# Performance work log

Measured on AMD Instinct MI355X. Metric: run time of the kernel, lower is better.

Reference implementation:

```python
import jax, jax.numpy as jnp
import numpy as np

N = 50000        # nodes
E = 1_600_000    # edges (avg degree 32)
H = 4            # attention heads
DPH = 32         # dims per head
D = H * DPH      # hidden/output dim = 128
IN_DIM = 5
NEG_SLOPE = 0.2
LN_EPS = 1e-5


def _glorot(key, shape):
    fan_in = shape[0] if len(shape) > 1 else shape[-1]
    return jax.random.normal(key, shape, jnp.float32) / jnp.sqrt(jnp.float32(fan_in))


def setup_inputs() -> dict:
    key = jax.random.key(0)
    ks = jax.random.split(key, 24)
    inp = {
        'x': jax.random.normal(ks[0], (N, IN_DIM), jnp.float32),
        'w_in': _glorot(ks[1], (IN_DIM, D)),
        'b_in': jnp.zeros((D,), jnp.float32),
    }
    for i in range(3):
        k = 2 + 6 * i
        inp[f'w{i}'] = _glorot(ks[k], (D, D))            # GAT linear
        inp[f'asrc{i}'] = _glorot(ks[k + 1], (H, DPH))   # att_src
        inp[f'adst{i}'] = _glorot(ks[k + 2], (H, DPH))   # att_dst
        inp[f'cb{i}'] = jnp.zeros((D,), jnp.float32)     # conv bias
        inp[f'g{i}'] = jnp.ones((D,), jnp.float32)       # LN gamma
        inp[f'lb{i}'] = jnp.zeros((D,), jnp.float32)     # LN beta
    inp['edge_index'] = jax.random.randint(ks[23], (2, E), 0, N, dtype=jnp.int32)
    return inp


def _gat_layer(h, src, dst, W, a_src, a_dst, bias):
    # h: [N, D]; src/dst: [E+N] (self loops included)
    xh = (h @ W).reshape(N, H, DPH)                      # [N, H, DPH]
    al_s = jnp.einsum('nhd,hd->nh', xh, a_src)           # [N, H]
    al_d = jnp.einsum('nhd,hd->nh', xh, a_dst)
    e = jax.nn.leaky_relu(al_s[src] + al_d[dst], NEG_SLOPE)   # [E', H]
    m = jax.ops.segment_max(e, dst, num_segments=N)      # segment softmax over incoming edges
    ex = jnp.exp(e - m[dst])
    denom = jax.ops.segment_sum(ex, dst, num_segments=N)
    alpha = ex / (denom[dst] + 1e-16)                    # [E', H]
    out = jax.ops.segment_sum(xh[src] * alpha[..., None], dst, num_segments=N)
    return out.reshape(N, D) + bias


def _layer_norm(x, g, b):
    mu = jnp.mean(x, axis=-1, keepdims=True)
    var = jnp.mean((x - mu) ** 2, axis=-1, keepdims=True)
    return (x - mu) * jax.lax.rsqrt(var + LN_EPS) * g + b


def reference(x, w_in, b_in,
              w0, asrc0, adst0, cb0, g0, lb0,
              w1, asrc1, adst1, cb1, g1, lb1,
              w2, asrc2, adst2, cb2, g2, lb2,
              edge_index):
    loops = jnp.arange(N, dtype=edge_index.dtype)
    src = jnp.concatenate([edge_index[0], loops])        # PyG GATConv add_self_loops=True
    dst = jnp.concatenate([edge_index[1], loops])
    h = x @ w_in + b_in                                  # [N, D]
    layers = [(w0, asrc0, adst0, cb0, g0, lb0),
              (w1, asrc1, adst1, cb1, g1, lb1),
              (w2, asrc2, adst2, cb2, g2, lb2)]
    for i, (W, a_s, a_d, cb, g, lb) in enumerate(layers):
        h_new = _gat_layer(h, src, dst, W, a_s, a_d, cb)
        h_new = _layer_norm(h_new, g, lb)
        if i < 2:
            h_new = jax.nn.relu(h_new)                   # dropout = identity in eval
        h = h + h_new                                    # dims always match (128)
    return h
```

## Files before the change

kernel.cpp:

```cpp
#include <hip/hip_runtime.h>

#define NN 50000
#define NE 1600000
#define EP (NE + NN)
#define D 128
#define H 4
#define NEG 0.2f
#define LN_EPS 1e-5f
#define NBUCK 49
#define BCAP 40960
#define CHUNK 4096

typedef _Float16 f16;
typedef _Float16 half8 __attribute__((ext_vector_type(8)));
typedef _Float16 half2v __attribute__((ext_vector_type(2)));
typedef float f32x4v __attribute__((ext_vector_type(4)));
typedef unsigned short u16;
typedef unsigned int u32;

static __device__ __forceinline__ float leakyf(float v) { return fmaxf(v, NEG * v); }

static __device__ __forceinline__ int fkey(float v) {
    int b = __float_as_int(v);
    return b >= 0 ? b : (b ^ 0x7fffffff);
}
static __device__ __forceinline__ float fdec(int k) {
    return __int_as_float(k >= 0 ? k : (k ^ 0x7fffffff));
}
#define NEG_INF_KEY 0x807fffff

__global__ void k_init(int* __restrict__ deg, int* __restrict__ gmaxk,
                       int* __restrict__ gcur,
                       const float* __restrict__ w0, const float* __restrict__ w1,
                       const float* __restrict__ w2, f16* __restrict__ wt,
                       const float* __restrict__ as0, const float* __restrict__ ad0,
                       const float* __restrict__ as1, const float* __restrict__ ad1,
                       const float* __restrict__ as2, const float* __restrict__ ad2,
                       f16* __restrict__ ws16) {
    int t = blockIdx.x * blockDim.x + threadIdx.x;
    if (t < NN) deg[t] = 0;
    if (t < 12) gmaxk[t] = NEG_INF_KEY;
    if (t < NBUCK) gcur[t] = 0;
    int u = t - 50176;
    if (u >= 0 && u < 3 * D * D) {
        int l = u / (D * D), rem = u % (D * D);
        int k = rem >> 7, c = rem & 127;
        const float* w = (l == 0) ? w0 : (l == 1) ? w1 : w2;
        wt[l * D * D + c * D + k] = (f16)w[rem];
    }
    int v = t - 99328;
    if (v >= 0 && v < 3 * 16 * D) {
        int l = v / (16 * D), rem = v % (16 * D);
        int c = rem >> 7, k = rem & 127;
        f16 out = (f16)0.f;
        if (c < 8) {
            int head = c >> 1;
            const float* w = (l == 0) ? w0 : (l == 1) ? w1 : w2;
            const float* av = (c & 1) ? ((l == 0) ? ad0 : (l == 1) ? ad1 : ad2)
                                      : ((l == 0) ? as0 : (l == 1) ? as1 : as2);
            float s = 0.f;
#pragma unroll
            for (int j = 0; j < 32; j++)
                s = fmaf(w[k * D + head * 32 + j], av[head * 32 + j], s);
            out = (f16)s;
        }
        ws16[l * 16 * D + c * D + k] = out;
    }
}

__global__ __launch_bounds__(256) void k_bin(const int* __restrict__ ei,
                                             int* __restrict__ gcur,
                                             u32* __restrict__ binned) {
    __shared__ u32 pk[CHUNK];
    __shared__ int hist[NBUCK], base[NBUCK], lcur[NBUCK];
    int tid = threadIdx.x;
    int cbase = blockIdx.x * CHUNK;
    if (tid < NBUCK) hist[tid] = 0;
    __syncthreads();
#pragma unroll
    for (int j = 0; j < CHUNK / 256; j++) {
        int k = cbase + j * 256 + tid;
        u32 v = 0xFFFFFFFFu;
        if (k < EP) {
            int src, dst;
            if (k < NE) { src = ei[k]; dst = ei[NE + k]; }
            else        { src = k - NE; dst = src; }
            v = ((u32)dst << 16) | (u32)src;
            atomicAdd(&hist[dst >> 10], 1);
        }
        pk[j * 256 + tid] = v;
    }
    __syncthreads();
    if (tid < NBUCK) {
        base[tid] = atomicAdd(&gcur[tid], hist[tid]);
        lcur[tid] = 0;
    }
    __syncthreads();
#pragma unroll
    for (int j = 0; j < CHUNK / 256; j++) {
        u32 v = pk[j * 256 + tid];
        if (v != 0xFFFFFFFFu) {
            int b = v >> 26;
            int pos = base[b] + atomicAdd(&lcur[b], 1);
            binned[(size_t)b * BCAP + pos] = v;
        }
    }
}

__global__ __launch_bounds__(1024) void k_cnt2(const int* __restrict__ gcur,
                                               const u32* __restrict__ binned,
                                               int* __restrict__ deg) {
    __shared__ int hist[1024];
    int b = blockIdx.x >> 2, sub = blockIdx.x & 3;
    hist[threadIdx.x] = 0;
    __syncthreads();
    int cnt = gcur[b];
    const u32* bb = binned + (size_t)b * BCAP;
    for (int i = sub * 1024 + threadIdx.x; i < cnt; i += 4096)
        atomicAdd(&hist[(bb[i] >> 16) & 1023], 1);
    __syncthreads();
    int n = (b << 10) + threadIdx.x;
    if (n < NN && hist[threadIdx.x]) atomicAdd(&deg[n], hist[threadIdx.x]);
}

#define SCAN_B 512
__global__ void k_scan1(const int* __restrict__ deg, int* __restrict__ stmp, int* __restrict__ bsum) {
    __shared__ int sm[SCAN_B];
    int i = blockIdx.x * SCAN_B + threadIdx.x;
    sm[threadIdx.x] = (i < NN) ? ((deg[i] + 3) & ~3) : 0;
    __syncthreads();
    for (int off = 1; off < SCAN_B; off <<= 1) {
        int t = (threadIdx.x >= off) ? sm[threadIdx.x - off] : 0;
        __syncthreads();
        sm[threadIdx.x] += t;
        __syncthreads();
    }
    if (i < NN) stmp[i] = sm[threadIdx.x];
    if (threadIdx.x == SCAN_B - 1) bsum[blockIdx.x] = sm[SCAN_B - 1];
}

__global__ void k_scan2(int* __restrict__ bsum, int nb) {
    __shared__ int sm[256];
    int v = (threadIdx.x < nb) ? bsum[threadIdx.x] : 0;
    sm[threadIdx.x] = v;
    __syncthreads();
    for (int off = 1; off < 256; off <<= 1) {
        int t = (threadIdx.x >= off) ? sm[threadIdx.x - off] : 0;
        __syncthreads();
        sm[threadIdx.x] += t;
        __syncthreads();
    }
    if (threadIdx.x < nb) bsum[threadIdx.x] = sm[threadIdx.x];
}

__global__ void k_scan3(const int* __restrict__ stmp, const int* __restrict__ bsum, int* __restrict__ rowptr) {
    int i = blockIdx.x * SCAN_B + threadIdx.x;
    if (i >= NN) return;
    int add = (blockIdx.x > 0) ? bsum[blockIdx.x - 1] : 0;
    rowptr[i + 1] = stmp[i] + add;
    if (i == 0) rowptr[0] = 0;
}

__global__ void k_pad(const int* __restrict__ rowptr, const int* __restrict__ deg,
                      int* __restrict__ cur, u16* __restrict__ csr) {
    int i = blockIdx.x * blockDim.x + threadIdx.x;
    if (i >= NN) return;
    int rp = rowptr[i];
    cur[i] = rp;
    int d = deg[i];
    int ad = (d + 3) & ~3;
    for (int j = d; j < ad; ++j) csr[rp + j] = 0xFFFFu;
}

__global__ __launch_bounds__(1024) void k_scatter(const int* __restrict__ gcur,
                                                  int* __restrict__ cur,
                                                  const u32* __restrict__ binned,
                                                  u16* __restrict__ csr) {
    int b = blockIdx.x >> 2, sub = blockIdx.x & 3;
    int cnt = gcur[b];
    const u32* bb = binned + (size_t)b * BCAP;
    for (int i = sub * 1024 + threadIdx.x; i < cnt; i += 4096) {
        u32 v = bb[i];
        int dst = v >> 16;
        int pos = atomicAdd(&cur[dst], 1);
        csr[pos] = (u16)(v & 0xFFFFu);
    }
}

__global__ void k_in(const float* __restrict__ x, const float* __restrict__ w,
                     const float* __restrict__ b, f16* __restrict__ h16) {
    int t = blockIdx.x * blockDim.x + threadIdx.x;
    if (t >= NN * D) return;
    int n = t >> 7, d = t & 127;
    const float* xr = x + n * 5;
    float acc = b[d];
#pragma unroll
    for (int k = 0; k < 5; k++) acc = fmaf(xr[k], w[k * D + d], acc);
    h16[t] = (f16)acc;
}

__global__ __launch_bounds__(256) void k_gemm(const f16* __restrict__ h16,
                                              const f16* __restrict__ wt,
                                              const f16* __restrict__ ws16,
                                              f16* __restrict__ xh,
                                              float* __restrict__ als,
                                              float* __restrict__ ald,
                                              int* __restrict__ gmaxk) {
    __shared__ int sgk[4];
    if (threadIdx.x < 4) sgk[threadIdx.x] = NEG_INF_KEY;
    int wid = threadIdx.x >> 6;
    int lane = threadIdx.x & 63;
    int wbase = blockIdx.x * 128 + wid * 32;
    int r = lane & 15;
    int g = lane >> 4;

    int arow0 = wbase + r;      if (arow0 >= NN) arow0 = NN - 1;
    int arow1 = wbase + 16 + r; if (arow1 >= NN) arow1 = NN - 1;
    const f16* a0p = h16 + (size_t)arow0 * D + g * 8;
    const f16* a1p = h16 + (size_t)arow1 * D + g * 8;

    f32x4v acc0[8], acc1[8], al0, al1;
#pragma unroll
    for (int nt = 0; nt < 8; nt++) {
        acc0[nt] = (f32x4v){0.f, 0.f, 0.f, 0.f};
        acc1[nt] = (f32x4v){0.f, 0.f, 0.f, 0.f};
    }
    al0 = (f32x4v){0.f, 0.f, 0.f, 0.f};
    al1 = (f32x4v){0.f, 0.f, 0.f, 0.f};

#pragma unroll
    for (int ks = 0; ks < 4; ks++) {
        half8 a0 = *(const half8*)(a0p + ks * 32);
        half8 a1 = *(const half8*)(a1p + ks * 32);
        half8 bal = *(const half8*)(ws16 + (size_t)r * D + ks * 32 + g * 8);
        al0 = __builtin_amdgcn_mfma_f32_16x16x32_f16(a0, bal, al0, 0, 0, 0);
        al1 = __builtin_amdgcn_mfma_f32_16x16x32_f16(a1, bal, al1, 0, 0, 0);
#pragma unroll
        for (int nt = 0; nt < 8; nt++) {
            half8 b = *(const half8*)(wt + (size_t)(nt * 16 + r) * D + ks * 32 + g * 8);
            acc0[nt] = __builtin_amdgcn_mfma_f32_16x16x32_f16(a0, b, acc0[nt], 0, 0, 0);
            acc1[nt] = __builtin_amdgcn_mfma_f32_16x16x32_f16(a1, b, acc1[nt], 0, 0, 0);
        }
    }

#pragma unroll
    for (int rg = 0; rg < 4; rg++) {
        int n0 = wbase + g * 4 + rg;
        if (n0 < NN) {
#pragma unroll
            for (int nt = 0; nt < 8; nt++)
                xh[(size_t)n0 * D + nt * 16 + r] = (f16)acc0[nt][rg];
        }
        int n1 = wbase + 16 + g * 4 + rg;
        if (n1 < NN) {
#pragma unroll
            for (int nt = 0; nt < 8; nt++)
                xh[(size_t)n1 * D + nt * 16 + r] = (f16)acc1[nt][rg];
        }
    }

    float m = -1e30f;
#pragma unroll
    for (int rg = 0; rg < 4; rg++) {
        int n0 = wbase + g * 4 + rg;
        int n1 = wbase + 16 + g * 4 + rg;
        float v0 = al0[rg], v1 = al1[rg];
        if (r < 8) {
            int hh = r >> 1;
            if (r & 1) {
                if (n0 < NN) ald[n0 * H + hh] = v0;
                if (n1 < NN) ald[n1 * H + hh] = v1;
            } else {
                if (n0 < NN) als[n0 * H + hh] = v0;
                if (n1 < NN) als[n1 * H + hh] = v1;
                m = fmaxf(m, fmaxf(v0, v1));
            }
        }
    }
    m = fmaxf(m, __shfl_xor(m, 16));
    m = fmaxf(m, __shfl_xor(m, 32));
    __syncthreads();
    if (lane < 8 && !(r & 1)) atomicMax(&sgk[r >> 1], fkey(m));
    __syncthreads();
    if (threadIdx.x < 4) atomicMax(&gmaxk[threadIdx.x], sgk[threadIdx.x]);
}

__global__ __launch_bounds__(256) void k_agg(const f16* __restrict__ xh,
                                             const float* __restrict__ als,
                                             const float* __restrict__ ald,
                                             const int* __restrict__ gmaxk,
                                             const int* __restrict__ rowptr,
                                             const u16* __restrict__ csr,
                                             const float* __restrict__ cb,
                                             const float* __restrict__ gamma,
                                             const float* __restrict__ beta,
                                             f16* __restrict__ h16,
                                             float* __restrict__ hout, int do_relu) {
    int node = blockIdx.x * 4 + (threadIdx.x >> 6);
    if (node >= NN) return;
    int lane = threadIdx.x & 63;
    int slot = lane >> 4;
    int q = lane & 15;
    int head = q >> 2;

    int start = rowptr[node], end = rowptr[node + 1];

    float adH = ald[node * H + head];
    float mH = leakyf(fdec(gmaxk[head]) + adH);

    float acc[8];
#pragma unroll
    for (int j = 0; j < 8; j++) acc[j] = 0.f;
    float den = 0.f;

    int sh = (slot & 1) << 4;
    bool hiw = (slot & 2) != 0;

#pragma unroll 4
    for (int e = start; e < end; e += 4) {
        uint2 cw = *(const uint2*)(csr + e);
        unsigned dw = hiw ? cw.y : cw.x;
        unsigned s = (dw >> sh) & 0xffffu;
        bool valid = s != 0xffffu;
        unsigned sc = valid ? s : 0u;
        float al = als[sc * H + head];
        float ev = valid ? __expf(leakyf(al + adH) - mH) : 0.f;
        den += ev;
        half8 p = *(const half8*)(xh + sc * D + q * 8);
#pragma unroll
        for (int j = 0; j < 8; j++) acc[j] = fmaf(ev, (float)p[j], acc[j]);
    }

    den += __shfl_xor(den, 16);
    den += __shfl_xor(den, 32);
#pragma unroll
    for (int j = 0; j < 8; j++) {
        acc[j] += __shfl_xor(acc[j], 16);
        acc[j] += __shfl_xor(acc[j], 32);
    }

    float inv_den = 1.f / (den + 1e-16f);
    float o[8];
    const float4* cb4 = (const float4*)(cb + q * 8);
    float4 cba = cb4[0], cbb = cb4[1];
    o[0] = fmaf(acc[0], inv_den, cba.x);
    o[1] = fmaf(acc[1], inv_den, cba.y);
    o[2] = fmaf(acc[2], inv_den, cba.z);
    o[3] = fmaf(acc[3], inv_den, cba.w);
    o[4] = fmaf(acc[4], inv_den, cbb.x);
    o[5] = fmaf(acc[5], inv_den, cbb.y);
    o[6] = fmaf(acc[6], inv_den, cbb.z);
    o[7] = fmaf(acc[7], inv_den, cbb.w);

    float s = 0.f;
#pragma unroll
    for (int j = 0; j < 8; j++) s += o[j];
#pragma unroll
    for (int off = 1; off < 16; off <<= 1) s += __shfl_xor(s, off);
    float mean = s * (1.f / 128.f);
    float v = 0.f;
    float c[8];
#pragma unroll
    for (int j = 0; j < 8; j++) { c[j] = o[j] - mean; v = fmaf(c[j], c[j], v); }
#pragma unroll
    for (int off = 1; off < 16; off <<= 1) v += __shfl_xor(v, off);
    float inv = rsqrtf(v * (1.f / 128.f) + LN_EPS);

    int dim = q * 8 + slot * 2;
    float2 g2 = *(const float2*)(gamma + dim);
    float2 b2 = *(const float2*)(beta + dim);
    float r0 = c[slot * 2] * inv * g2.x + b2.x;
    float r1 = c[slot * 2 + 1] * inv * g2.y + b2.y;
    if (do_relu) { r0 = fmaxf(r0, 0.f); r1 = fmaxf(r1, 0.f); }
    half2v hv16 = *(const half2v*)&h16[(size_t)node * D + dim];
    float n0 = (float)hv16[0] + r0;
    float n1 = (float)hv16[1] + r1;
    if (do_relu) {
        half2v h2; h2[0] = (f16)n0; h2[1] = (f16)n1;
        *(half2v*)&h16[(size_t)node * D + dim] = h2;
    } else {
        float2* hp = (float2*)&hout[(size_t)node * D + dim];
        *hp = (float2){n0, n1};
    }
}

extern "C" void kernel_launch(void* const* d_in, const int* in_sizes, int n_in,
                              void* d_out, int out_size, void* d_ws, size_t ws_size,
                              hipStream_t stream) {
    const float* x    = (const float*)d_in[0];
    const float* w_in = (const float*)d_in[1];
    const float* b_in = (const float*)d_in[2];
    const int*   ei   = (const int*)d_in[21];
    float* hout = (float*)d_out;

    char* w = (char*)d_ws;
    int* deg    = (int*)w;  w += (size_t)NN * 4;
    int* cur    = (int*)w;  w += (size_t)NN * 4;
    int* stmp   = (int*)w;  w += (size_t)NN * 4;
    int* bsum   = (int*)w;  w += 1024;
    int* rowptr = (int*)w;  w += (size_t)(NN + 4) * 4;
    int* gmaxk  = (int*)w;  w += 64;
    int* gcur   = (int*)w;  w += 256;
    u16* csr    = (u16*)w;  w += (size_t)(EP + 3 * NN + 16) * 2;
    f16* h16    = (f16*)w;  w += (size_t)NN * D * 2;
    f16* xh     = (f16*)w;  w += (size_t)NN * D * 2;
    f16* wt     = (f16*)w;  w += (size_t)3 * D * D * 2;
    f16* ws16   = (f16*)w;  w += (size_t)3 * 16 * D * 2;
    float* als  = (float*)w; w += (size_t)NN * H * 4;
    float* ald  = (float*)w; w += (size_t)NN * H * 4;
    u32* binned = (u32*)h16;

    k_init<<<412, 256, 0, stream>>>(deg, gmaxk, gcur,
                                    (const float*)d_in[3], (const float*)d_in[9],
                                    (const float*)d_in[15], wt,
                                    (const float*)d_in[4], (const float*)d_in[5],
                                    (const float*)d_in[10], (const float*)d_in[11],
                                    (const float*)d_in[16], (const float*)d_in[17],
                                    ws16);
    k_bin<<<(EP + CHUNK - 1) / CHUNK, 256, 0, stream>>>(ei, gcur, binned);
    k_cnt2<<<NBUCK * 4, 1024, 0, stream>>>(gcur, binned, deg);
    int nbScan = (NN + SCAN_B - 1) / SCAN_B;
    k_scan1<<<nbScan, SCAN_B, 0, stream>>>(deg, stmp, bsum);
    k_scan2<<<1, 256, 0, stream>>>(bsum, nbScan);
    k_scan3<<<nbScan, SCAN_B, 0, stream>>>(stmp, bsum, rowptr);
    k_pad<<<(NN + 255) / 256, 256, 0, stream>>>(rowptr, deg, cur, csr);
    k_scatter<<<NBUCK * 4, 1024, 0, stream>>>(gcur, cur, binned, csr);

    k_in<<<(NN * D) / 256, 256, 0, stream>>>(x, w_in, b_in, h16);

    for (int L = 0; L < 3; ++L) {
        const float* cb   = (const float*)d_in[6 + 6 * L];
        const float* g    = (const float*)d_in[7 + 6 * L];
        const float* lb   = (const float*)d_in[8 + 6 * L];
        k_gemm<<<(NN + 127) / 128, 256, 0, stream>>>(h16, wt + (size_t)L * D * D,
                                                     ws16 + (size_t)L * 16 * D,
                                                     xh, als, ald, gmaxk + 4 * L);
        k_agg<<<NN / 4, 256, 0, stream>>>(xh, als, ald, gmaxk + 4 * L, rowptr, csr,
                                          cb, g, lb, h16, hout, L < 2 ? 1 : 0);
    }
}
```

Measured before the change: 411.6 us.

## Partition CSR by source chunk and aggregate multiple nodes per wave chunk-wise

```diff
diff --git a/kernel.cpp b/kernel.cpp
--- a/kernel.cpp
+++ b/kernel.cpp
@@ -10,9 +10,14 @@
 #define NBUCK 49
 #define BCAP 40960
 #define CHUNK 4096
+#define NCHUNK 8
+#define CSH 13
+#define NSEG (NN * NCHUNK)
+#define NPW 8
 
 typedef _Float16 f16;
 typedef _Float16 half8 __attribute__((ext_vector_type(8)));
+typedef _Float16 half4 __attribute__((ext_vector_type(4)));
 typedef _Float16 half2v __attribute__((ext_vector_type(2)));
 typedef float f32x4v __attribute__((ext_vector_type(4)));
 typedef unsigned short u16;
@@ -29,7 +34,7 @@
 }
 #define NEG_INF_KEY 0x807fffff
 
-__global__ void k_init(int* __restrict__ deg, int* __restrict__ gmaxk,
+__global__ void k_init(int* __restrict__ deg8, int* __restrict__ gmaxk,
                        int* __restrict__ gcur,
                        const float* __restrict__ w0, const float* __restrict__ w1,
                        const float* __restrict__ w2, f16* __restrict__ wt,
@@ -38,7 +43,7 @@
                        const float* __restrict__ as2, const float* __restrict__ ad2,
                        f16* __restrict__ ws16) {
     int t = blockIdx.x * blockDim.x + threadIdx.x;
-    if (t < NN) deg[t] = 0;
+    if (t < NSEG) deg8[t] = 0;
     if (t < 12) gmaxk[t] = NEG_INF_KEY;
     if (t < NBUCK) gcur[t] = 0;
     int u = t - 50176;
@@ -109,25 +114,34 @@
 
 __global__ __launch_bounds__(1024) void k_cnt2(const int* __restrict__ gcur,
                                                const u32* __restrict__ binned,
-                                               int* __restrict__ deg) {
-    __shared__ int hist[1024];
+                                               int* __restrict__ deg8) {
+    __shared__ int hist[1024 * NCHUNK];
     int b = blockIdx.x >> 2, sub = blockIdx.x & 3;
-    hist[threadIdx.x] = 0;
+#pragma unroll
+    for (int j = 0; j < NCHUNK; j++) hist[j * 1024 + threadIdx.x] = 0;
     __syncthreads();
     int cnt = gcur[b];
     const u32* bb = binned + (size_t)b * BCAP;
-    for (int i = sub * 1024 + threadIdx.x; i < cnt; i += 4096)
-        atomicAdd(&hist[(bb[i] >> 16) & 1023], 1);
-    __syncthreads();
-    int n = (b << 10) + threadIdx.x;
-    if (n < NN && hist[threadIdx.x]) atomicAdd(&deg[n], hist[threadIdx.x]);
-}
-
-#define SCAN_B 512
-__global__ void k_scan1(const int* __restrict__ deg, int* __restrict__ stmp, int* __restrict__ bsum) {
+    for (int i = sub * 1024 + threadIdx.x; i < cnt; i += 4096) {
+        u32 v = bb[i];
+        int idx = (int)((v >> 16) & 1023) * NCHUNK + (int)((v & 0xffffu) >> CSH);
+        atomicAdd(&hist[idx], 1);
+    }
+    __syncthreads();
+    int nb0 = b << 10;
+    for (int i = threadIdx.x; i < 1024 * NCHUNK; i += 1024) {
+        int node = nb0 + (i >> 3);
+        int hv = hist[i];
+        if (node < NN && hv) atomicAdd(&deg8[node * NCHUNK + (i & 7)], hv);
+    }
+}
+
+#define SCAN_B 1024
+__global__ __launch_bounds__(1024) void k_scan1(const int* __restrict__ deg8,
+                                                int* __restrict__ stmp, int* __restrict__ bsum) {
     __shared__ int sm[SCAN_B];
     int i = blockIdx.x * SCAN_B + threadIdx.x;
-    sm[threadIdx.x] = (i < NN) ? ((deg[i] + 3) & ~3) : 0;
+    sm[threadIdx.x] = (i < NSEG) ? ((deg8[i] + 1) & ~1) : 0;
     __syncthreads();
     for (int off = 1; off < SCAN_B; off <<= 1) {
         int t = (threadIdx.x >= off) ? sm[threadIdx.x - off] : 0;
@@ -135,16 +149,16 @@
         sm[threadIdx.x] += t;
         __syncthreads();
     }
-    if (i < NN) stmp[i] = sm[threadIdx.x];
+    if (i < NSEG) stmp[i] = sm[threadIdx.x];
     if (threadIdx.x == SCAN_B - 1) bsum[blockIdx.x] = sm[SCAN_B - 1];
 }
 
-__global__ void k_scan2(int* __restrict__ bsum, int nb) {
-    __shared__ int sm[256];
+__global__ __launch_bounds__(1024) void k_scan2(int* __restrict__ bsum, int nb) {
+    __shared__ int sm[1024];
     int v = (threadIdx.x < nb) ? bsum[threadIdx.x] : 0;
     sm[threadIdx.x] = v;
     __syncthreads();
-    for (int off = 1; off < 256; off <<= 1) {
+    for (int off = 1; off < 1024; off <<= 1) {
         int t = (threadIdx.x >= off) ? sm[threadIdx.x - off] : 0;
         __syncthreads();
         sm[threadIdx.x] += t;
@@ -153,22 +167,23 @@
     if (threadIdx.x < nb) bsum[threadIdx.x] = sm[threadIdx.x];
 }
 
-__global__ void k_scan3(const int* __restrict__ stmp, const int* __restrict__ bsum, int* __restrict__ rowptr) {
+__global__ __launch_bounds__(1024) void k_scan3(const int* __restrict__ stmp,
+                                                const int* __restrict__ bsum, int* __restrict__ rowptr) {
     int i = blockIdx.x * SCAN_B + threadIdx.x;
-    if (i >= NN) return;
+    if (i >= NSEG) return;
     int add = (blockIdx.x > 0) ? bsum[blockIdx.x - 1] : 0;
     rowptr[i + 1] = stmp[i] + add;
     if (i == 0) rowptr[0] = 0;
 }
 
-__global__ void k_pad(const int* __restrict__ rowptr, const int* __restrict__ deg,
+__global__ void k_pad(const int* __restrict__ rowptr, const int* __restrict__ deg8,
                       int* __restrict__ cur, u16* __restrict__ csr) {
     int i = blockIdx.x * blockDim.x + threadIdx.x;
-    if (i >= NN) return;
+    if (i >= NSEG) return;
     int rp = rowptr[i];
     cur[i] = rp;
-    int d = deg[i];
-    int ad = (d + 3) & ~3;
+    int d = deg8[i];
+    int ad = (d + 1) & ~1;
     for (int j = d; j < ad; ++j) csr[rp + j] = 0xFFFFu;
 }
 
@@ -182,8 +197,9 @@
     for (int i = sub * 1024 + threadIdx.x; i < cnt; i += 4096) {
         u32 v = bb[i];
         int dst = v >> 16;
-        int pos = atomicAdd(&cur[dst], 1);
-        csr[pos] = (u16)(v & 0xFFFFu);
+        int src = v & 0xffffu;
+        int pos = atomicAdd(&cur[dst * NCHUNK + (src >> CSH)], 1);
+        csr[pos] = (u16)src;
     }
 }
 
@@ -285,102 +301,111 @@
     if (threadIdx.x < 4) atomicMax(&gmaxk[threadIdx.x], sgk[threadIdx.x]);
 }
 
-__global__ __launch_bounds__(256) void k_agg(const f16* __restrict__ xh,
-                                             const float* __restrict__ als,
-                                             const float* __restrict__ ald,
-                                             const int* __restrict__ gmaxk,
-                                             const int* __restrict__ rowptr,
-                                             const u16* __restrict__ csr,
-                                             const float* __restrict__ cb,
-                                             const float* __restrict__ gamma,
-                                             const float* __restrict__ beta,
-                                             f16* __restrict__ h16,
-                                             float* __restrict__ hout, int do_relu) {
-    int node = blockIdx.x * 4 + (threadIdx.x >> 6);
-    if (node >= NN) return;
+__global__ __launch_bounds__(256, 6) void k_agg(const f16* __restrict__ xh,
+                                                const float* __restrict__ als,
+                                                const float* __restrict__ ald,
+                                                const int* __restrict__ gmaxk,
+                                                const int* __restrict__ rp,
+                                                const u16* __restrict__ csr,
+                                                const float* __restrict__ cb,
+                                                const float* __restrict__ gamma,
+                                                const float* __restrict__ beta,
+                                                f16* __restrict__ h16,
+                                                float* __restrict__ hout, int do_relu) {
+    int wid = threadIdx.x >> 6;
     int lane = threadIdx.x & 63;
-    int slot = lane >> 4;
-    int q = lane & 15;
-    int head = q >> 2;
-
-    int start = rowptr[node], end = rowptr[node + 1];
-
-    float adH = ald[node * H + head];
-    float mH = leakyf(fdec(gmaxk[head]) + adH);
-
-    float acc[8];
-#pragma unroll
-    for (int j = 0; j < 8; j++) acc[j] = 0.f;
-    float den = 0.f;
-
-    int sh = (slot & 1) << 4;
-    bool hiw = (slot & 2) != 0;
-
-#pragma unroll 4
-    for (int e = start; e < end; e += 4) {
-        uint2 cw = *(const uint2*)(csr + e);
-        unsigned dw = hiw ? cw.y : cw.x;
-        unsigned s = (dw >> sh) & 0xffffu;
-        bool valid = s != 0xffffu;
-        unsigned sc = valid ? s : 0u;
-        float al = als[sc * H + head];
-        float ev = valid ? __expf(leakyf(al + adH) - mH) : 0.f;
-        den += ev;
-        half8 p = *(const half8*)(xh + sc * D + q * 8);
-#pragma unroll
-        for (int j = 0; j < 8; j++) acc[j] = fmaf(ev, (float)p[j], acc[j]);
-    }
-
-    den += __shfl_xor(den, 16);
-    den += __shfl_xor(den, 32);
-#pragma unroll
-    for (int j = 0; j < 8; j++) {
-        acc[j] += __shfl_xor(acc[j], 16);
-        acc[j] += __shfl_xor(acc[j], 32);
-    }
-
-    float inv_den = 1.f / (den + 1e-16f);
-    float o[8];
-    const float4* cb4 = (const float4*)(cb + q * 8);
-    float4 cba = cb4[0], cbb = cb4[1];
-    o[0] = fmaf(acc[0], inv_den, cba.x);
-    o[1] = fmaf(acc[1], inv_den, cba.y);
-    o[2] = fmaf(acc[2], inv_den, cba.z);
-    o[3] = fmaf(acc[3], inv_den, cba.w);
-    o[4] = fmaf(acc[4], inv_den, cbb.x);
-    o[5] = fmaf(acc[5], inv_den, cbb.y);
-    o[6] = fmaf(acc[6], inv_den, cbb.z);
-    o[7] = fmaf(acc[7], inv_den, cbb.w);
-
-    float s = 0.f;
-#pragma unroll
-    for (int j = 0; j < 8; j++) s += o[j];
-#pragma unroll
-    for (int off = 1; off < 16; off <<= 1) s += __shfl_xor(s, off);
-    float mean = s * (1.f / 128.f);
-    float v = 0.f;
-    float c[8];
-#pragma unroll
-    for (int j = 0; j < 8; j++) { c[j] = o[j] - mean; v = fmaf(c[j], c[j], v); }
-#pragma unroll
-    for (int off = 1; off < 16; off <<= 1) v += __shfl_xor(v, off);
-    float inv = rsqrtf(v * (1.f / 128.f) + LN_EPS);
-
-    int dim = q * 8 + slot * 2;
-    float2 g2 = *(const float2*)(gamma + dim);
-    float2 b2 = *(const float2*)(beta + dim);
-    float r0 = c[slot * 2] * inv * g2.x + b2.x;
-    float r1 = c[slot * 2 + 1] * inv * g2.y + b2.y;
-    if (do_relu) { r0 = fmaxf(r0, 0.f); r1 = fmaxf(r1, 0.f); }
-    half2v hv16 = *(const half2v*)&h16[(size_t)node * D + dim];
-    float n0 = (float)hv16[0] + r0;
-    float n1 = (float)hv16[1] + r1;
-    if (do_relu) {
-        half2v h2; h2[0] = (f16)n0; h2[1] = (f16)n1;
-        *(half2v*)&h16[(size_t)node * D + dim] = h2;
-    } else {
-        float2* hp = (float2*)&hout[(size_t)node * D + dim];
-        *hp = (float2){n0, n1};
+    int nbase = (blockIdx.x * 4 + wid) * NPW;
+    int slot = lane >> 5;
+    int q = lane & 31;
+    int head = q >> 3;
+    int sh = slot << 4;
+
+    float acc[NPW][4];
+    float den[NPW];
+#pragma unroll
+    for (int n = 0; n < NPW; n++) {
+        den[n] = 0.f;
+        acc[n][0] = acc[n][1] = acc[n][2] = acc[n][3] = 0.f;
+    }
+
+    float gm = fdec(gmaxk[head]);
+
+    for (int p = 0; p < 7; ++p) {
+#pragma unroll
+        for (int n = 0; n < NPW; n++) {
+            int node = nbase + n;
+            if (node >= NN) continue;
+            float adH = ald[node * H + head];
+            float mH = leakyf(gm + adH);
+            int seg = node * NCHUNK + p;
+            int s0 = rp[seg], s1 = rp[seg + 1];
+            for (int e = s0; e < s1; e += 2) {
+                u32 cw = *(const u32*)(csr + e);
+                unsigned s = (cw >> sh) & 0xffffu;
+                bool valid = s != 0xffffu;
+                unsigned sc = valid ? s : 0u;
+                float al = als[sc * H + head];
+                float ev = valid ? __expf(leakyf(al + adH) - mH) : 0.f;
+                den[n] += ev;
+                half4 pv = *(const half4*)(xh + (size_t)sc * D + q * 4);
+                acc[n][0] = fmaf(ev, (float)pv[0], acc[n][0]);
+                acc[n][1] = fmaf(ev, (float)pv[1], acc[n][1]);
+                acc[n][2] = fmaf(ev, (float)pv[2], acc[n][2]);
+                acc[n][3] = fmaf(ev, (float)pv[3], acc[n][3]);
+            }
+        }
+    }
+
+    float4 cb4 = ((const float4*)cb)[q];
+    float4 g4 = ((const float4*)gamma)[q];
+    float4 b4 = ((const float4*)beta)[q];
+
+#pragma unroll
+    for (int n = 0; n < NPW; n++) {
+        int node = nbase + n;
+        if (node >= NN) continue;
+        float d = den[n] + __shfl_xor(den[n], 32);
+        float o0 = acc[n][0] + __shfl_xor(acc[n][0], 32);
+        float o1 = acc[n][1] + __shfl_xor(acc[n][1], 32);
+        float o2 = acc[n][2] + __shfl_xor(acc[n][2], 32);
+        float o3 = acc[n][3] + __shfl_xor(acc[n][3], 32);
+        float inv_den = 1.f / (d + 1e-16f);
+        o0 = fmaf(o0, inv_den, cb4.x);
+        o1 = fmaf(o1, inv_den, cb4.y);
+        o2 = fmaf(o2, inv_den, cb4.z);
+        o3 = fmaf(o3, inv_den, cb4.w);
+
+        float s = o0 + o1 + o2 + o3;
+#pragma unroll
+        for (int off = 1; off < 32; off <<= 1) s += __shfl_xor(s, off);
+        float mean = s * (1.f / 128.f);
+        float c0 = o0 - mean, c1 = o1 - mean, c2 = o2 - mean, c3 = o3 - mean;
+        float v = c0 * c0 + c1 * c1 + c2 * c2 + c3 * c3;
+#pragma unroll
+        for (int off = 1; off < 32; off <<= 1) v += __shfl_xor(v, off);
+        float inv = rsqrtf(v * (1.f / 128.f) + LN_EPS);
+
+        float r0 = c0 * inv * g4.x + b4.x;
+        float r1 = c1 * inv * g4.y + b4.y;
+        float r2 = c2 * inv * g4.z + b4.z;
+        float r3 = c3 * inv * g4.w + b4.w;
+        if (do_relu) {
+            r0 = fmaxf(r0, 0.f); r1 = fmaxf(r1, 0.f);
+            r2 = fmaxf(r2, 0.f); r3 = fmaxf(r3, 0.f);
+        }
+        if (slot == 0) {
+            half4 hv = *(const half4*)&h16[(size_t)node * D + q * 4];
+            float n0 = (float)hv[0] + r0;
+            float n1 = (float)hv[1] + r1;
+            float n2 = (float)hv[2] + r2;
+            float n3 = (float)hv[3] + r3;
+            if (do_relu) {
+                half4 h2; h2[0] = (f16)n0; h2[1] = (f16)n1; h2[2] = (f16)n2; h2[3] = (f16)n3;
+                *(half4*)&h16[(size_t)node * D + q * 4] = h2;
+            } else {
+                *(float4*)&hout[(size_t)node * D + q * 4] = (float4){n0, n1, n2, n3};
+            }
+        }
     }
 }
 
@@ -394,14 +419,14 @@
     float* hout = (float*)d_out;
 
     char* w = (char*)d_ws;
-    int* deg    = (int*)w;  w += (size_t)NN * 4;
-    int* cur    = (int*)w;  w += (size_t)NN * 4;
-    int* stmp   = (int*)w;  w += (size_t)NN * 4;
-    int* bsum   = (int*)w;  w += 1024;
-    int* rowptr = (int*)w;  w += (size_t)(NN + 4) * 4;
+    int* deg8   = (int*)w;  w += (size_t)NSEG * 4;
+    int* cur    = (int*)w;  w += (size_t)NSEG * 4;
+    int* stmp   = (int*)w;  w += (size_t)NSEG * 4;
+    int* bsum   = (int*)w;  w += 4096;
+    int* rowptr = (int*)w;  w += (size_t)(NSEG + 8) * 4;
     int* gmaxk  = (int*)w;  w += 64;
     int* gcur   = (int*)w;  w += 256;
-    u16* csr    = (u16*)w;  w += (size_t)(EP + 3 * NN + 16) * 2;
+    u16* csr    = (u16*)w;  w += (size_t)(EP + NSEG + 64) * 2;
     f16* h16    = (f16*)w;  w += (size_t)NN * D * 2;
     f16* xh     = (f16*)w;  w += (size_t)NN * D * 2;
     f16* wt     = (f16*)w;  w += (size_t)3 * D * D * 2;
@@ -410,24 +435,25 @@
     float* ald  = (float*)w; w += (size_t)NN * H * 4;
     u32* binned = (u32*)h16;
 
-    k_init<<<412, 256, 0, stream>>>(deg, gmaxk, gcur,
-                                    (const float*)d_in[3], (const float*)d_in[9],
-                                    (const float*)d_in[15], wt,
-                                    (const float*)d_in[4], (const float*)d_in[5],
-                                    (const float*)d_in[10], (const float*)d_in[11],
-                                    (const float*)d_in[16], (const float*)d_in[17],
-                                    ws16);
+    k_init<<<1563, 256, 0, stream>>>(deg8, gmaxk, gcur,
+                                     (const float*)d_in[3], (const float*)d_in[9],
+                                     (const float*)d_in[15], wt,
+                                     (const float*)d_in[4], (const float*)d_in[5],
+                                     (const float*)d_in[10], (const float*)d_in[11],
+                                     (const float*)d_in[16], (const float*)d_in[17],
+                                     ws16);
     k_bin<<<(EP + CHUNK - 1) / CHUNK, 256, 0, stream>>>(ei, gcur, binned);
-    k_cnt2<<<NBUCK * 4, 1024, 0, stream>>>(gcur, binned, deg);
-    int nbScan = (NN + SCAN_B - 1) / SCAN_B;
-    k_scan1<<<nbScan, SCAN_B, 0, stream>>>(deg, stmp, bsum);
-    k_scan2<<<1, 256, 0, stream>>>(bsum, nbScan);
+    k_cnt2<<<NBUCK * 4, 1024, 0, stream>>>(gcur, binned, deg8);
+    int nbScan = (NSEG + SCAN_B - 1) / SCAN_B;
+    k_scan1<<<nbScan, SCAN_B, 0, stream>>>(deg8, stmp, bsum);
+    k_scan2<<<1, 1024, 0, stream>>>(bsum, nbScan);
     k_scan3<<<nbScan, SCAN_B, 0, stream>>>(stmp, bsum, rowptr);
-    k_pad<<<(NN + 255) / 256, 256, 0, stream>>>(rowptr, deg, cur, csr);
+    k_pad<<<(NSEG + 255) / 256, 256, 0, stream>>>(rowptr, deg8, cur, csr);
     k_scatter<<<NBUCK * 4, 1024, 0, stream>>>(gcur, cur, binned, csr);
 
     k_in<<<(NN * D) / 256, 256, 0, stream>>>(x, w_in, b_in, h16);
 
+    int aggBlocks = (NN + 4 * NPW - 1) / (4 * NPW);
     for (int L = 0; L < 3; ++L) {
         const float* cb   = (const float*)d_in[6 + 6 * L];
         const float* g    = (const float*)d_in[7 + 6 * L];
@@ -435,7 +461,7 @@
         k_gemm<<<(NN + 127) / 128, 256, 0, stream>>>(h16, wt + (size_t)L * D * D,
                                                      ws16 + (size_t)L * 16 * D,
                                                      xh, als, ald, gmaxk + 4 * L);
-        k_agg<<<NN / 4, 256, 0, stream>>>(xh, als, ald, gmaxk + 4 * L, rowptr, csr,
-                                          cb, g, lb, h16, hout, L < 2 ? 1 : 0);
-    }
-}
+        k_agg<<<aggBlocks, 256, 0, stream>>>(xh, als, ald, gmaxk + 4 * L, rowptr, csr,
+                                             cb, g, lb, h16, hout, L < 2 ? 1 : 0);
+    }
+}
```

Measured after the change: 1.054 ms. +156.0%, slower.

## Split each node's CSR row into source-range segments for gather locality

Applied to the files above, without the earlier changes.

```diff
diff --git a/kernel.cpp b/kernel.cpp
--- a/kernel.cpp
+++ b/kernel.cpp
@@ -10,6 +10,9 @@
 #define NBUCK 49
 #define BCAP 40960
 #define CHUNK 4096
+#define NCHUNK 4
+#define CSH 14
+#define NSEG (NN * NCHUNK)
 
 typedef _Float16 f16;
 typedef _Float16 half8 __attribute__((ext_vector_type(8)));
@@ -38,7 +41,7 @@
                        const float* __restrict__ as2, const float* __restrict__ ad2,
                        f16* __restrict__ ws16) {
     int t = blockIdx.x * blockDim.x + threadIdx.x;
-    if (t < NN) deg[t] = 0;
+    if (t < NSEG) deg[t] = 0;
     if (t < 12) gmaxk[t] = NEG_INF_KEY;
     if (t < NBUCK) gcur[t] = 0;
     int u = t - 50176;
@@ -110,24 +113,33 @@
 __global__ __launch_bounds__(1024) void k_cnt2(const int* __restrict__ gcur,
                                                const u32* __restrict__ binned,
                                                int* __restrict__ deg) {
-    __shared__ int hist[1024];
+    __shared__ int hist[4096];
     int b = blockIdx.x >> 2, sub = blockIdx.x & 3;
-    hist[threadIdx.x] = 0;
+#pragma unroll
+    for (int j = 0; j < 4; j++) hist[j * 1024 + threadIdx.x] = 0;
     __syncthreads();
     int cnt = gcur[b];
     const u32* bb = binned + (size_t)b * BCAP;
-    for (int i = sub * 1024 + threadIdx.x; i < cnt; i += 4096)
-        atomicAdd(&hist[(bb[i] >> 16) & 1023], 1);
-    __syncthreads();
-    int n = (b << 10) + threadIdx.x;
-    if (n < NN && hist[threadIdx.x]) atomicAdd(&deg[n], hist[threadIdx.x]);
-}
-
-#define SCAN_B 512
-__global__ void k_scan1(const int* __restrict__ deg, int* __restrict__ stmp, int* __restrict__ bsum) {
+    for (int i = sub * 1024 + threadIdx.x; i < cnt; i += 4096) {
+        u32 v = bb[i];
+        int idx = (int)((v >> 16) & 1023) * 4 + (int)((v & 0xffffu) >> CSH);
+        atomicAdd(&hist[idx], 1);
+    }
+    __syncthreads();
+    int segBase = b << 12;
+    for (int i = threadIdx.x; i < 4096; i += 1024) {
+        int seg = segBase + i;
+        int hv = hist[i];
+        if (seg < NSEG && hv) atomicAdd(&deg[seg], hv);
+    }
+}
+
+#define SCAN_B 1024
+__global__ __launch_bounds__(1024) void k_scan1(const int* __restrict__ deg,
+                                                int* __restrict__ stmp, int* __restrict__ bsum) {
     __shared__ int sm[SCAN_B];
     int i = blockIdx.x * SCAN_B + threadIdx.x;
-    sm[threadIdx.x] = (i < NN) ? ((deg[i] + 3) & ~3) : 0;
+    sm[threadIdx.x] = (i < NSEG) ? ((deg[i] + 3) & ~3) : 0;
     __syncthreads();
     for (int off = 1; off < SCAN_B; off <<= 1) {
         int t = (threadIdx.x >= off) ? sm[threadIdx.x - off] : 0;
@@ -135,7 +147,7 @@
         sm[threadIdx.x] += t;
         __syncthreads();
     }
-    if (i < NN) stmp[i] = sm[threadIdx.x];
+    if (i < NSEG) stmp[i] = sm[threadIdx.x];
     if (threadIdx.x == SCAN_B - 1) bsum[blockIdx.x] = sm[SCAN_B - 1];
 }
 
@@ -153,23 +165,23 @@
     if (threadIdx.x < nb) bsum[threadIdx.x] = sm[threadIdx.x];
 }
 
-__global__ void k_scan3(const int* __restrict__ stmp, const int* __restrict__ bsum, int* __restrict__ rowptr) {
+__global__ __launch_bounds__(1024) void k_scan3(const int* __restrict__ stmp,
+                                                const int* __restrict__ bsum,
+                                                const int* __restrict__ deg,
+                                                int* __restrict__ rowptr,
+                                                int* __restrict__ cur,
+                                                u16* __restrict__ csr) {
     int i = blockIdx.x * SCAN_B + threadIdx.x;
-    if (i >= NN) return;
+    if (i >= NSEG) return;
     int add = (blockIdx.x > 0) ? bsum[blockIdx.x - 1] : 0;
-    rowptr[i + 1] = stmp[i] + add;
+    int end = stmp[i] + add;
+    rowptr[i + 1] = end;
     if (i == 0) rowptr[0] = 0;
-}
-
-__global__ void k_pad(const int* __restrict__ rowptr, const int* __restrict__ deg,
-                      int* __restrict__ cur, u16* __restrict__ csr) {
-    int i = blockIdx.x * blockDim.x + threadIdx.x;
-    if (i >= NN) return;
-    int rp = rowptr[i];
-    cur[i] = rp;
     int d = deg[i];
     int ad = (d + 3) & ~3;
-    for (int j = d; j < ad; ++j) csr[rp + j] = 0xFFFFu;
+    int start = end - ad;
+    cur[i] = start;
+    for (int j = start + d; j < end; ++j) csr[j] = 0xFFFFu;
 }
 
 __global__ __launch_bounds__(1024) void k_scatter(const int* __restrict__ gcur,
@@ -182,8 +194,9 @@
     for (int i = sub * 1024 + threadIdx.x; i < cnt; i += 4096) {
         u32 v = bb[i];
         int dst = v >> 16;
-        int pos = atomicAdd(&cur[dst], 1);
-        csr[pos] = (u16)(v & 0xFFFFu);
+        int src = v & 0xffffu;
+        int pos = atomicAdd(&cur[dst * NCHUNK + (src >> CSH)], 1);
+        csr[pos] = (u16)src;
     }
 }
 
@@ -289,7 +302,7 @@
                                              const float* __restrict__ als,
                                              const float* __restrict__ ald,
                                              const int* __restrict__ gmaxk,
-                                             const int* __restrict__ rowptr,
+                                             const int* __restrict__ rp,
                                              const u16* __restrict__ csr,
                                              const float* __restrict__ cb,
                                              const float* __restrict__ gamma,
@@ -303,7 +316,9 @@
     int q = lane & 15;
     int head = q >> 2;
 
-    int start = rowptr[node], end = rowptr[node + 1];
+    int4 rp4 = ((const int4*)rp)[node];
+    int e4 = rp[node * 4 + 4];
+    int starts[5] = {rp4.x, rp4.y, rp4.z, rp4.w, e4};
 
     float adH = ald[node * H + head];
     float mH = leakyf(fdec(gmaxk[head]) + adH);
@@ -316,19 +331,23 @@
     int sh = (slot & 1) << 4;
     bool hiw = (slot & 2) != 0;
 
-#pragma unroll 4
-    for (int e = start; e < end; e += 4) {
-        uint2 cw = *(const uint2*)(csr + e);
-        unsigned dw = hiw ? cw.y : cw.x;
-        unsigned s = (dw >> sh) & 0xffffu;
-        bool valid = s != 0xffffu;
-        unsigned sc = valid ? s : 0u;
-        float al = als[sc * H + head];
-        float ev = valid ? __expf(leakyf(al + adH) - mH) : 0.f;
-        den += ev;
-        half8 p = *(const half8*)(xh + sc * D + q * 8);
-#pragma unroll
-        for (int j = 0; j < 8; j++) acc[j] = fmaf(ev, (float)p[j], acc[j]);
+#pragma unroll
+    for (int p = 0; p < 4; ++p) {
+        int s0 = starts[p], s1 = starts[p + 1];
+#pragma unroll 2
+        for (int e = s0; e < s1; e += 4) {
+            uint2 cw = *(const uint2*)(csr + e);
+            unsigned dw = hiw ? cw.y : cw.x;
+            unsigned s = (dw >> sh) & 0xffffu;
+            bool valid = s != 0xffffu;
+            unsigned sc = valid ? s : 0u;
+            float al = als[sc * H + head];
+            float ev = valid ? __expf(leakyf(al + adH) - mH) : 0.f;
+            den += ev;
+            half8 pv = *(const half8*)(xh + sc * D + q * 8);
+#pragma unroll
+            for (int j = 0; j < 8; j++) acc[j] = fmaf(ev, (float)pv[j], acc[j]);
+        }
     }
 
     den += __shfl_xor(den, 16);
@@ -394,14 +413,14 @@
     float* hout = (float*)d_out;
 
     char* w = (char*)d_ws;
-    int* deg    = (int*)w;  w += (size_t)NN * 4;
-    int* cur    = (int*)w;  w += (size_t)NN * 4;
-    int* stmp   = (int*)w;  w += (size_t)NN * 4;
+    int* deg    = (int*)w;  w += (size_t)NSEG * 4;
+    int* cur    = (int*)w;  w += (size_t)NSEG * 4;
+    int* stmp   = (int*)w;  w += (size_t)NSEG * 4;
     int* bsum   = (int*)w;  w += 1024;
-    int* rowptr = (int*)w;  w += (size_t)(NN + 4) * 4;
+    int* rowptr = (int*)w;  w += (size_t)(NSEG + 8) * 4;
     int* gmaxk  = (int*)w;  w += 64;
     int* gcur   = (int*)w;  w += 256;
-    u16* csr    = (u16*)w;  w += (size_t)(EP + 3 * NN + 16) * 2;
+    u16* csr    = (u16*)w;  w += (size_t)(EP + 3 * NSEG + 64) * 2;
     f16* h16    = (f16*)w;  w += (size_t)NN * D * 2;
     f16* xh     = (f16*)w;  w += (size_t)NN * D * 2;
     f16* wt     = (f16*)w;  w += (size_t)3 * D * D * 2;
@@ -410,7 +429,7 @@
     float* ald  = (float*)w; w += (size_t)NN * H * 4;
     u32* binned = (u32*)h16;
 
-    k_init<<<412, 256, 0, stream>>>(deg, gmaxk, gcur,
+    k_init<<<(NSEG + 255) / 256, 256, 0, stream>>>(deg, gmaxk, gcur,
                                     (const float*)d_in[3], (const float*)d_in[9],
                                     (const float*)d_in[15], wt,
                                     (const float*)d_in[4], (const float*)d_in[5],
@@ -419,11 +438,10 @@
                                     ws16);
     k_bin<<<(EP + CHUNK - 1) / CHUNK, 256, 0, stream>>>(ei, gcur, binned);
     k_cnt2<<<NBUCK * 4, 1024, 0, stream>>>(gcur, binned, deg);
-    int nbScan = (NN + SCAN_B - 1) / SCAN_B;
+    int nbScan = (NSEG + SCAN_B - 1) / SCAN_B;
     k_scan1<<<nbScan, SCAN_B, 0, stream>>>(deg, stmp, bsum);
     k_scan2<<<1, 256, 0, stream>>>(bsum, nbScan);
-    k_scan3<<<nbScan, SCAN_B, 0, stream>>>(stmp, bsum, rowptr);
-    k_pad<<<(NN + 255) / 256, 256, 0, stream>>>(rowptr, deg, cur, csr);
+    k_scan3<<<nbScan, SCAN_B, 0, stream>>>(stmp, bsum, deg, rowptr, cur, csr);
     k_scatter<<<NBUCK * 4, 1024, 0, stream>>>(gcur, cur, binned, csr);
 
     k_in<<<(NN * D) / 256, 256, 0, stream>>>(x, w_in, b_in, h16);
@@ -435,7 +453,7 @@
         k_gemm<<<(NN + 127) / 128, 256, 0, stream>>>(h16, wt + (size_t)L * D * D,
                                                      ws16 + (size_t)L * 16 * D,
                                                      xh, als, ald, gmaxk + 4 * L);
-        k_agg<<<NN / 4, 256, 0, stream>>>(xh, als, ald, gmaxk + 4 * L, rowptr, csr,
-                                          cb, g, lb, h16, hout, L < 2 ? 1 : 0);
-    }
-}
+        k_agg<<<(NN + 3) / 4, 256, 0, stream>>>(xh, als, ald, gmaxk + 4 * L, rowptr, csr,
+                                                cb, g, lb, h16, hout, L < 2 ? 1 : 0);
+    }
+}
```

Measured after the change: 418.0 us. About the same (+1.5%).

## Process two nodes per wavefront in aggregation and fuse padding into scan

Applied to the files above, without the earlier changes.

```diff
diff --git a/kernel.cpp b/kernel.cpp
--- a/kernel.cpp
+++ b/kernel.cpp
@@ -153,23 +153,19 @@
     if (threadIdx.x < nb) bsum[threadIdx.x] = sm[threadIdx.x];
 }
 
-__global__ void k_scan3(const int* __restrict__ stmp, const int* __restrict__ bsum, int* __restrict__ rowptr) {
+__global__ void k_scan3(const int* __restrict__ stmp, const int* __restrict__ bsum,
+                        const int* __restrict__ deg, int* __restrict__ rowptr,
+                        int* __restrict__ cur, u16* __restrict__ csr) {
     int i = blockIdx.x * SCAN_B + threadIdx.x;
     if (i >= NN) return;
     int add = (blockIdx.x > 0) ? bsum[blockIdx.x - 1] : 0;
-    rowptr[i + 1] = stmp[i] + add;
+    int end = stmp[i] + add;
+    rowptr[i + 1] = end;
     if (i == 0) rowptr[0] = 0;
-}
-
-__global__ void k_pad(const int* __restrict__ rowptr, const int* __restrict__ deg,
-                      int* __restrict__ cur, u16* __restrict__ csr) {
-    int i = blockIdx.x * blockDim.x + threadIdx.x;
-    if (i >= NN) return;
-    int rp = rowptr[i];
-    cur[i] = rp;
     int d = deg[i];
-    int ad = (d + 3) & ~3;
-    for (int j = d; j < ad; ++j) csr[rp + j] = 0xFFFFu;
+    int start = end - ((d + 3) & ~3);
+    cur[i] = start;
+    for (int j = start + d; j < end; ++j) csr[j] = 0xFFFFu;
 }
 
 __global__ __launch_bounds__(1024) void k_scatter(const int* __restrict__ gcur,
@@ -289,98 +285,120 @@
                                              const float* __restrict__ als,
                                              const float* __restrict__ ald,
                                              const int* __restrict__ gmaxk,
-                                             const int* __restrict__ rowptr,
+                                             const int* __restrict__ rp,
                                              const u16* __restrict__ csr,
                                              const float* __restrict__ cb,
                                              const float* __restrict__ gamma,
                                              const float* __restrict__ beta,
                                              f16* __restrict__ h16,
                                              float* __restrict__ hout, int do_relu) {
-    int node = blockIdx.x * 4 + (threadIdx.x >> 6);
-    if (node >= NN) return;
+    int pair = blockIdx.x * 4 + (threadIdx.x >> 6);
+    if (pair * 2 >= NN) return;
+    int nodeA = pair * 2, nodeB = pair * 2 + 1;
     int lane = threadIdx.x & 63;
     int slot = lane >> 4;
     int q = lane & 15;
     int head = q >> 2;
-
-    int start = rowptr[node], end = rowptr[node + 1];
-
-    float adH = ald[node * H + head];
-    float mH = leakyf(fdec(gmaxk[head]) + adH);
-
-    float acc[8];
-#pragma unroll
-    for (int j = 0; j < 8; j++) acc[j] = 0.f;
-    float den = 0.f;
+    unsigned qo = q * 8;
+
+    int eA = rp[nodeA], endA = rp[nodeA + 1], endB = rp[nodeB + 1];
+    int eB = endA;
+
+    float gm = fdec(gmaxk[head]);
+    float adA = ald[nodeA * H + head];
+    float adB = ald[nodeB * H + head];
+    float mA = leakyf(gm + adA);
+    float mB = leakyf(gm + adB);
+
+    float accA[8], accB[8];
+#pragma unroll
+    for (int j = 0; j < 8; j++) { accA[j] = 0.f; accB[j] = 0.f; }
+    float denA = 0.f, denB = 0.f;
 
     int sh = (slot & 1) << 4;
     bool hiw = (slot & 2) != 0;
 
-#pragma unroll 4
-    for (int e = start; e < end; e += 4) {
-        uint2 cw = *(const uint2*)(csr + e);
-        unsigned dw = hiw ? cw.y : cw.x;
-        unsigned s = (dw >> sh) & 0xffffu;
-        bool valid = s != 0xffffu;
-        unsigned sc = valid ? s : 0u;
-        float al = als[sc * H + head];
-        float ev = valid ? __expf(leakyf(al + adH) - mH) : 0.f;
-        den += ev;
-        half8 p = *(const half8*)(xh + sc * D + q * 8);
-#pragma unroll
-        for (int j = 0; j < 8; j++) acc[j] = fmaf(ev, (float)p[j], acc[j]);
-    }
-
-    den += __shfl_xor(den, 16);
-    den += __shfl_xor(den, 32);
-#pragma unroll
-    for (int j = 0; j < 8; j++) {
-        acc[j] += __shfl_xor(acc[j], 16);
-        acc[j] += __shfl_xor(acc[j], 32);
-    }
-
-    float inv_den = 1.f / (den + 1e-16f);
-    float o[8];
-    const float4* cb4 = (const float4*)(cb + q * 8);
-    float4 cba = cb4[0], cbb = cb4[1];
-    o[0] = fmaf(acc[0], inv_den, cba.x);
-    o[1] = fmaf(acc[1], inv_den, cba.y);
-    o[2] = fmaf(acc[2], inv_den, cba.z);
-    o[3] = fmaf(acc[3], inv_den, cba.w);
-    o[4] = fmaf(acc[4], inv_den, cbb.x);
-    o[5] = fmaf(acc[5], inv_den, cbb.y);
-    o[6] = fmaf(acc[6], inv_den, cbb.z);
-    o[7] = fmaf(acc[7], inv_den, cbb.w);
-
-    float s = 0.f;
-#pragma unroll
-    for (int j = 0; j < 8; j++) s += o[j];
-#pragma unroll
-    for (int off = 1; off < 16; off <<= 1) s += __shfl_xor(s, off);
-    float mean = s * (1.f / 128.f);
-    float v = 0.f;
-    float c[8];
-#pragma unroll
-    for (int j = 0; j < 8; j++) { c[j] = o[j] - mean; v = fmaf(c[j], c[j], v); }
-#pragma unroll
-    for (int off = 1; off < 16; off <<= 1) v += __shfl_xor(v, off);
-    float inv = rsqrtf(v * (1.f / 128.f) + LN_EPS);
-
+#define AGG_BODY(E, AD, M, DEN, ACC)                                          \
+    {                                                                          \
+        uint2 cw = *(const uint2*)(csr + (E));                                 \
+        unsigned dw = hiw ? cw.y : cw.x;                                       \
+        unsigned s = (dw >> sh) & 0xffffu;                                     \
+        bool valid = s != 0xffffu;                                             \
+        unsigned sc = valid ? s : 0u;                                          \
+        float al = als[sc * 4u + (unsigned)head];                              \
+        float ev = valid ? __expf(leakyf(al + (AD)) - (M)) : 0.f;              \
+        DEN += ev;                                                             \
+        half8 pv = *(const half8*)(xh + sc * 128u + qo);                       \
+        _Pragma("unroll")                                                      \
+        for (int j = 0; j < 8; j++) ACC[j] = fmaf(ev, (float)pv[j], ACC[j]);   \
+    }
+
+    int nc = min((endA - eA) >> 2, (endB - eB) >> 2);
+    for (int i = 0; i < nc; ++i) {
+        AGG_BODY(eA, adA, mA, denA, accA)
+        AGG_BODY(eB, adB, mB, denB, accB)
+        eA += 4; eB += 4;
+    }
+    for (; eA < endA; eA += 4) AGG_BODY(eA, adA, mA, denA, accA)
+    for (; eB < endB; eB += 4) AGG_BODY(eB, adB, mB, denB, accB)
+#undef AGG_BODY
+
+    const float4* cb4p = (const float4*)(cb + q * 8);
+    float4 cba = cb4p[0], cbb = cb4p[1];
     int dim = q * 8 + slot * 2;
     float2 g2 = *(const float2*)(gamma + dim);
     float2 b2 = *(const float2*)(beta + dim);
-    float r0 = c[slot * 2] * inv * g2.x + b2.x;
-    float r1 = c[slot * 2 + 1] * inv * g2.y + b2.y;
-    if (do_relu) { r0 = fmaxf(r0, 0.f); r1 = fmaxf(r1, 0.f); }
-    half2v hv16 = *(const half2v*)&h16[(size_t)node * D + dim];
-    float n0 = (float)hv16[0] + r0;
-    float n1 = (float)hv16[1] + r1;
-    if (do_relu) {
-        half2v h2; h2[0] = (f16)n0; h2[1] = (f16)n1;
-        *(half2v*)&h16[(size_t)node * D + dim] = h2;
-    } else {
-        float2* hp = (float2*)&hout[(size_t)node * D + dim];
-        *hp = (float2){n0, n1};
+
+#pragma unroll
+    for (int which = 0; which < 2; ++which) {
+        float* acc = which ? accB : accA;
+        float den = which ? denB : denA;
+        int node = which ? nodeB : nodeA;
+
+        den += __shfl_xor(den, 16);
+        den += __shfl_xor(den, 32);
+#pragma unroll
+        for (int j = 0; j < 8; j++) {
+            acc[j] += __shfl_xor(acc[j], 16);
+            acc[j] += __shfl_xor(acc[j], 32);
+        }
+        float inv_den = 1.f / (den + 1e-16f);
+        float o[8];
+        o[0] = fmaf(acc[0], inv_den, cba.x);
+        o[1] = fmaf(acc[1], inv_den, cba.y);
+        o[2] = fmaf(acc[2], inv_den, cba.z);
+        o[3] = fmaf(acc[3], inv_den, cba.w);
+        o[4] = fmaf(acc[4], inv_den, cbb.x);
+        o[5] = fmaf(acc[5], inv_den, cbb.y);
+        o[6] = fmaf(acc[6], inv_den, cbb.z);
+        o[7] = fmaf(acc[7], inv_den, cbb.w);
+
+        float s = 0.f;
+#pragma unroll
+        for (int j = 0; j < 8; j++) s += o[j];
+#pragma unroll
+        for (int off = 1; off < 16; off <<= 1) s += __shfl_xor(s, off);
+        float mean = s * (1.f / 128.f);
+        float v = 0.f;
+        float c[8];
+#pragma unroll
+        for (int j = 0; j < 8; j++) { c[j] = o[j] - mean; v = fmaf(c[j], c[j], v); }
+#pragma unroll
+        for (int off = 1; off < 16; off <<= 1) v += __shfl_xor(v, off);
+        float inv = rsqrtf(v * (1.f / 128.f) + LN_EPS);
+
+        float r0 = c[slot * 2] * inv * g2.x + b2.x;
+        float r1 = c[slot * 2 + 1] * inv * g2.y + b2.y;
+        if (do_relu) { r0 = fmaxf(r0, 0.f); r1 = fmaxf(r1, 0.f); }
+        half2v hv16 = *(const half2v*)&h16[(size_t)node * D + dim];
+        float n0 = (float)hv16[0] + r0;
+        float n1 = (float)hv16[1] + r1;
+        if (do_relu) {
+            half2v h2; h2[0] = (f16)n0; h2[1] = (f16)n1;
+            *(half2v*)&h16[(size_t)node * D + dim] = h2;
+        } else {
+            *(float2*)&hout[(size_t)node * D + dim] = (float2){n0, n1};
+        }
     }
 }
 
@@ -398,10 +416,10 @@
     int* cur    = (int*)w;  w += (size_t)NN * 4;
     int* stmp   = (int*)w;  w += (size_t)NN * 4;
     int* bsum   = (int*)w;  w += 1024;
-    int* rowptr = (int*)w;  w += (size_t)(NN + 4) * 4;
+    int* rowptr = (int*)w;  w += (size_t)(NN + 8) * 4;
     int* gmaxk  = (int*)w;  w += 64;
     int* gcur   = (int*)w;  w += 256;
-    u16* csr    = (u16*)w;  w += (size_t)(EP + 3 * NN + 16) * 2;
+    u16* csr    = (u16*)w;  w += (size_t)(EP + 3 * NN + 64) * 2;
     f16* h16    = (f16*)w;  w += (size_t)NN * D * 2;
     f16* xh     = (f16*)w;  w += (size_t)NN * D * 2;
     f16* wt     = (f16*)w;  w += (size_t)3 * D * D * 2;
@@ -422,12 +440,12 @@
     int nbScan = (NN + SCAN_B - 1) / SCAN_B;
     k_scan1<<<nbScan, SCAN_B, 0, stream>>>(deg, stmp, bsum);
     k_scan2<<<1, 256, 0, stream>>>(bsum, nbScan);
-    k_scan3<<<nbScan, SCAN_B, 0, stream>>>(stmp, bsum, rowptr);
-    k_pad<<<(NN + 255) / 256, 256, 0, stream>>>(rowptr, deg, cur, csr);
+    k_scan3<<<nbScan, SCAN_B, 0, stream>>>(stmp, bsum, deg, rowptr, cur, csr);
     k_scatter<<<NBUCK * 4, 1024, 0, stream>>>(gcur, cur, binned, csr);
 
     k_in<<<(NN * D) / 256, 256, 0, stream>>>(x, w_in, b_in, h16);
 
+    int aggBlocks = (NN / 2 + 3) / 4;
     for (int L = 0; L < 3; ++L) {
         const float* cb   = (const float*)d_in[6 + 6 * L];
         const float* g    = (const float*)d_in[7 + 6 * L];
@@ -435,7 +453,7 @@
         k_gemm<<<(NN + 127) / 128, 256, 0, stream>>>(h16, wt + (size_t)L * D * D,
                                                      ws16 + (size_t)L * 16 * D,
                                                      xh, als, ald, gmaxk + 4 * L);
-        k_agg<<<NN / 4, 256, 0, stream>>>(xh, als, ald, gmaxk + 4 * L, rowptr, csr,
-                                          cb, g, lb, h16, hout, L < 2 ? 1 : 0);
-    }
-}
+        k_agg<<<aggBlocks, 256, 0, stream>>>(xh, als, ald, gmaxk + 4 * L, rowptr, csr,
+                                             cb, g, lb, h16, hout, L < 2 ? 1 : 0);
+    }
+}
```

After: 429.2 us. 1.04x slower.
